# Performance work log

Measured on AMD Instinct MI355X. Metric: run time of the kernel, lower is better.

## Reference

```python
import jax, jax.numpy as jnp
import numpy as np

K = 20
HID = 64
NUM_CLASSES = 50
BIG = 1e10  # effectively-infinite distance for self-loop exclusion


def knn_idx(x, k):
    # x: [N, d] -> idx: [N, k] indices of k nearest neighbors in feature space (excluding self)
    sq = jnp.sum(x * x, axis=1)
    dist = sq[:, None] + sq[None, :] - 2.0 * (x @ x.T)  # [N, N]
    n = x.shape[0]
    dist = dist.at[jnp.arange(n), jnp.arange(n)].set(BIG)
    _, idx = jax.lax.top_k(-dist, k)
    return idx


def edge_conv(x, k, W, b):
    # DynamicEdgeConv: message = relu(Linear(cat[x_i, x_j - x_i])), aggr = max over k neighbors
    idx = knn_idx(x, k)                      # [N, k]
    xj = x[idx]                              # [N, k, d] neighbor gather
    xi = jnp.broadcast_to(x[:, None, :], xj.shape)
    feat = jnp.concatenate([xi, xj - xi], axis=-1)   # [N, k, 2d]
    h = jax.nn.relu(jnp.einsum('nkf,fo->nko', feat, W) + b)
    return jnp.max(h, axis=1)                # [N, out]


def setup_inputs() -> dict:
    key = jax.random.key(0)
    ks = jax.random.split(key, 16)
    def lin(kw, fan_in, fan_out):
        s = 1.0 / np.sqrt(fan_in)
        return jax.random.uniform(kw, (fan_in, fan_out), jnp.float32, -s, s)
    inp = {
        'x':  jax.random.normal(ks[0], (8192, 3), jnp.float32),
        'W1': lin(ks[1], 2 * 3, HID),      'b1': jnp.zeros((HID,), jnp.float32),
        'W2': lin(ks[2], 2 * HID, HID),    'b2': jnp.zeros((HID,), jnp.float32),
        'W3': lin(ks[3], 2 * HID, HID),    'b3': jnp.zeros((HID,), jnp.float32),
        'Wl': lin(ks[4], 3 * HID, 1024),   'bl': jnp.zeros((1024,), jnp.float32),
        'Wm1': lin(ks[5], 1024, 256),      'bm1': jnp.zeros((256,), jnp.float32),
        'Wm2': lin(ks[6], 256, 128),       'bm2': jnp.zeros((128,), jnp.float32),
        'Wo': lin(ks[7], 128, NUM_CLASSES),'bo': jnp.zeros((NUM_CLASSES,), jnp.float32),
    }
    return inp


def reference(x, W1, b1, W2, b2, W3, b3, Wl, bl, Wm1, bm1, Wm2, bm2, Wo, bo):
    x1 = edge_conv(x, K, W1, b1)     # [N, 64], kNN on raw 3-D points
    x2 = edge_conv(x1, K, W2, b2)    # [N, 64], kNN recomputed in feature space
    x3 = edge_conv(x2, K, W3, b3)    # [N, 64]
    h = jnp.concatenate([x1, x2, x3], axis=1)            # [N, 192]
    h = jax.nn.relu(h @ Wl + bl)                         # lin1: MLP([192, 1024])
    h = jax.nn.relu(h @ Wm1 + bm1)                       # MLP([1024, 256]) (dropout: eval mode)
    h = jax.nn.relu(h @ Wm2 + bm2)                       # MLP([256, 128])
    out = h @ Wo + bo                                    # final Linear
    return jax.nn.log_softmax(out, axis=-1)
```

## Files before the change

### kernel.cpp

```cpp
#include <hip/hip_runtime.h>
#include <math.h>

#define NPTS 8192
#define KNN 20
#define KPART 10
#define NLISTS 32

#define OFF_SQ   0
#define OFF_IDX  8192
#define OFF_A    172032
#define OFF_B    696320
#define OFF_CAT  1220608
#define OFF_H1   2793472
#define OFF_H2   11182080
#define OFF_PART OFF_H1
#define OFF_PACK (OFF_H1 + 5242880)
#define PACK_ELEMS 262144
#define OFF_WT   (OFF_H2 + 1572864)

typedef __attribute__((ext_vector_type(8))) short bf16x8;
typedef __attribute__((ext_vector_type(16))) float f32x16;

__device__ inline unsigned umed3(unsigned a, unsigned b, unsigned c) {
    unsigned d;
    asm("v_med3_u32 %0, %1, %2, %3" : "=v"(d) : "v"(a), "v"(b), "v"(c));
    return d;
}

__device__ inline unsigned short f2bf(float f) {
    unsigned u = __float_as_uint(f);
    u += 0x7FFFu + ((u >> 16) & 1u);
    return (unsigned short)(u >> 16);
}

__device__ inline void tsplit(float x, unsigned short& hi, unsigned short& lo) {
    unsigned u = __float_as_uint(x);
    hi = (unsigned short)(u >> 16);
    float d = x - __uint_as_float(u & 0xFFFF0000u);
    lo = (unsigned short)(__float_as_uint(d) >> 16);
}

__global__ __launch_bounds__(256)
void setup_kernel(const float* __restrict__ x, float* __restrict__ sq,
                  unsigned short* __restrict__ Xhi, unsigned short* __restrict__ Xlo,
                  unsigned short* __restrict__ Yhi, unsigned short* __restrict__ Ylo,
                  const float* __restrict__ Wl, const float* __restrict__ Wm1,
                  const float* __restrict__ Wm2,
                  unsigned short* __restrict__ WlT_hi, unsigned short* __restrict__ WlT_lo,
                  unsigned short* __restrict__ Wm1T_hi, unsigned short* __restrict__ Wm1T_lo,
                  unsigned short* __restrict__ Wm2T_hi, unsigned short* __restrict__ Wm2T_lo) {
    const int b = blockIdx.x;
    if (b < 1920) {
        const float* W; unsigned short *Thi, *Tlo; int t, K, nbits;
        if (b < 768)       { W = Wl;  Thi = WlT_hi;  Tlo = WlT_lo;  t = b * 256 + threadIdx.x;          K = 192;  nbits = 10; }
        else if (b < 1792) { W = Wm1; Thi = Wm1T_hi; Tlo = Wm1T_lo; t = (b - 768) * 256 + threadIdx.x;  K = 1024; nbits = 8; }
        else               { W = Wm2; Thi = Wm2T_hi; Tlo = Wm2T_lo; t = (b - 1792) * 256 + threadIdx.x; K = 256;  nbits = 7; }
        int nmask = (1 << nbits) - 1;
        int k = t >> nbits, n = t & nmask;
        float xx = W[t];
        unsigned short hi, lo;
        tsplit(xx, hi, lo);
        Thi[(size_t)n * K + k] = hi;
        Tlo[(size_t)n * K + k] = lo;
    } else if (b < 2176) {
        int t = ((b - 1920) * 256 + threadIdx.x) * 2;
        int n = t >> 4, k = t & 15;
        float xv[2];
        xv[0] = (k < 3) ? x[(size_t)n * 3 + k] : 0.f;
        xv[1] = (k + 1 < 3) ? x[(size_t)n * 3 + k + 1] : 0.f;
        ushort2 hx, lx, hy, ly;
        unsigned short* hxp = (unsigned short*)&hx;
        unsigned short* lxp = (unsigned short*)&lx;
        unsigned short* hyp = (unsigned short*)&hy;
        unsigned short* lyp = (unsigned short*)&ly;
        #pragma unroll
        for (int e = 0; e < 2; ++e) {
            float xx = xv[e];
            unsigned short hi = f2bf(xx);
            float hif = __uint_as_float((unsigned)hi << 16);
            unsigned short lo = f2bf(xx - hif);
            float y = -2.f * xx;
            unsigned short yhi = f2bf(y);
            float yhif = __uint_as_float((unsigned)yhi << 16);
            unsigned short ylo = f2bf(y - yhif);
            hxp[e] = hi; lxp[e] = lo; hyp[e] = yhi; lyp[e] = ylo;
        }
        *(ushort2*)&Xhi[t] = hx;
        *(ushort2*)&Xlo[t] = lx;
        *(ushort2*)&Yhi[t] = hy;
        *(ushort2*)&Ylo[t] = ly;
    } else {
        int n = (b - 2176) * 256 + threadIdx.x;
        float a = x[(size_t)n * 3], bb = x[(size_t)n * 3 + 1], c = x[(size_t)n * 3 + 2];
        sq[n] = fmaf(a, a, fmaf(bb, bb, c * c));
    }
}

#define NETP(key)                                                              \
    do {                                                                       \
        _Pragma("unroll")                                                      \
        for (int p = KPART - 1; p >= 1; --p)                                   \
            top[p] = umed3(key, top[p - 1], top[p]);                           \
        top[0] = min(top[0], key);                                             \
    } while (0)

#define PROCESS(Cv, j0base)                                                    \
    do {                                                                       \
        _Pragma("unroll")                                                      \
        for (int q = 0; q < 4; ++q) {                                          \
            _Pragma("unroll")                                                  \
            for (int t = 0; t < 4; ++t) {                                      \
                const int j = (j0base) + h * 4 + q * 8 + t;                    \
                float dd = fmaxf((Cv)[q * 4 + t], 0.f);                        \
                unsigned key = (__float_as_uint(dd) & 0xFFFFE000u) | (unsigned)j; \
                if (j == bi) key = 0xFFFFFFFFu;                                \
                NETP(key);                                                     \
            }                                                                  \
        }                                                                      \
    } while (0)

template<int KP>
__global__ __launch_bounds__(256, 2)
void knnA_mfma(const unsigned short* __restrict__ Yhi, const unsigned short* __restrict__ Ylo,
               const unsigned short* __restrict__ Xhi, const unsigned short* __restrict__ Xlo,
               const float* __restrict__ sq, unsigned int* __restrict__ part) {
    constexpr int NS = KP / 16;
    constexpr int NT = 8;
    const int wave = threadIdx.x >> 6, lane = threadIdx.x & 63;
    const int col = lane & 31;
    const int h   = lane >> 5;
    const int bi  = (blockIdx.x * 4 + wave) * 32 + col;
    const int jbase = blockIdx.y * 256;

    bf16x8 bhi[NS], blo[NS];
    #pragma unroll
    for (int s = 0; s < NS; ++s) {
        bhi[s] = *(const bf16x8*)&Xhi[(size_t)bi * KP + s * 16 + h * 8];
        blo[s] = *(const bf16x8*)&Xlo[(size_t)bi * KP + s * 16 + h * 8];
    }
    const float sqi = sq[bi];

    unsigned top[KPART];
    #pragma unroll
    for (int k = 0; k < KPART; ++k) top[k] = 0xFFFFFFFFu;

    bf16x8 fA[NS], fB[NS], lo[NS];
    f32x16 CCa, CCb;

    {
        const size_t a0 = (size_t)(jbase + col) * KP + h * 8;
        #pragma unroll
        for (int s = 0; s < NS; ++s)
            fA[s] = *(const bf16x8*)&Yhi[a0 + s * 16];
    }

    #pragma unroll 1
    for (int jt2 = 0; jt2 < NT; jt2 += 2) {
        const int j0 = jbase + jt2 * 32;
        const int aj = j0 + col;

        #pragma unroll
        for (int s = 0; s < NS; ++s)
            fB[s] = *(const bf16x8*)&Yhi[(size_t)(aj + 32) * KP + s * 16 + h * 8];
        #pragma unroll
        for (int s = 0; s < NS; ++s)
            lo[s] = *(const bf16x8*)&Ylo[(size_t)aj * KP + s * 16 + h * 8];
        float4 e0 = *(const float4*)&sq[j0 + h * 4];
        float4 e1 = *(const float4*)&sq[j0 + h * 4 + 8];
        float4 e2 = *(const float4*)&sq[j0 + h * 4 + 16];
        float4 e3 = *(const float4*)&sq[j0 + h * 4 + 24];

        if (jt2 > 0) PROCESS(CCb, j0 - 32);

        CCa[0] = sqi + e0.x; CCa[1] = sqi + e0.y; CCa[2]  = sqi + e0.z; CCa[3]  = sqi + e0.w;
        CCa[4] = sqi + e1.x; CCa[5] = sqi + e1.y; CCa[6]  = sqi + e1.z; CCa[7]  = sqi + e1.w;
        CCa[8] = sqi + e2.x; CCa[9] = sqi + e2.y; CCa[10] = sqi + e2.z; CCa[11] = sqi + e2.w;
        CCa[12] = sqi + e3.x; CCa[13] = sqi + e3.y; CCa[14] = sqi + e3.z; CCa[15] = sqi + e3.w;
        #pragma unroll
        for (int s = 0; s < NS; ++s) {
            CCa = __builtin_amdgcn_mfma_f32_32x32x16_bf16(fA[s], bhi[s], CCa, 0, 0, 0);
            CCa = __builtin_amdgcn_mfma_f32_32x32x16_bf16(fA[s], blo[s], CCa, 0, 0, 0);
            CCa = __builtin_amdgcn_mfma_f32_32x32x16_bf16(lo[s], bhi[s], CCa, 0, 0, 0);
        }

        if (jt2 + 2 < NT) {
            #pragma unroll
            for (int s = 0; s < NS; ++s)
                fA[s] = *(const bf16x8*)&Yhi[(size_t)(aj + 64) * KP + s * 16 + h * 8];
        }
        #pragma unroll
        for (int s = 0; s < NS; ++s)
            lo[s] = *(const bf16x8*)&Ylo[(size_t)(aj + 32) * KP + s * 16 + h * 8];
        float4 o0 = *(const float4*)&sq[j0 + 32 + h * 4];
        float4 o1 = *(const float4*)&sq[j0 + 32 + h * 4 + 8];
        float4 o2 = *(const float4*)&sq[j0 + 32 + h * 4 + 16];
        float4 o3 = *(const float4*)&sq[j0 + 32 + h * 4 + 24];

        PROCESS(CCa, j0);

        CCb[0] = sqi + o0.x; CCb[1] = sqi + o0.y; CCb[2]  = sqi + o0.z; CCb[3]  = sqi + o0.w;
        CCb[4] = sqi + o1.x; CCb[5] = sqi + o1.y; CCb[6]  = sqi + o1.z; CCb[7]  = sqi + o1.w;
        CCb[8] = sqi + o2.x; CCb[9] = sqi + o2.y; CCb[10] = sqi + o2.z; CCb[11] = sqi + o2.w;
        CCb[12] = sqi + o3.x; CCb[13] = sqi + o3.y; CCb[14] = sqi + o3.z; CCb[15] = sqi + o3.w;
        #pragma unroll
        for (int s = 0; s < NS; ++s) {
            CCb = __builtin_amdgcn_mfma_f32_32x32x16_bf16(fB[s], bhi[s], CCb, 0, 0, 0);
            CCb = __builtin_amdgcn_mfma_f32_32x32x16_bf16(fB[s], blo[s], CCb, 0, 0, 0);
            CCb = __builtin_amdgcn_mfma_f32_32x32x16_bf16(lo[s], bhi[s], CCb, 0, 0, 0);
        }
    }
    PROCESS(CCb, jbase + (NT - 1) * 32);

    {
        bool done = false;
        #pragma unroll
        for (int k = 0; k < KPART; ++k) {
            unsigned c = __shfl_xor(top[k], 32);
            if (!done) done = __all(c >= top[KPART - 1]);
            if (!done) NETP(c);
        }
    }

    if (h == 0) {
        unsigned* o = part + ((size_t)bi * NLISTS + blockIdx.y) * KPART;
        #pragma unroll
        for (int k = 0; k < KPART; ++k) o[k] = top[k];
    }
}

template<int D>
__global__ __launch_bounds__(256)
void knnBfeat_kernel(const unsigned int* __restrict__ part, int* __restrict__ idx_out,
                     const float* __restrict__ X, int stride, const float* __restrict__ W,
                     float* __restrict__ A, float* __restrict__ B) {
    const int wave = threadIdx.x >> 6, lane = threadIdx.x & 63;
    if (blockIdx.x < 1024) {
        const int half = lane >> 5;
        const int l = lane & 31;
        const int row = (blockIdx.x * 4 + wave) * 2 + half;

        unsigned top[KNN];
        const unsigned* p = part + ((size_t)row * NLISTS + l) * KPART;
        {
            uint4 v0 = *(const uint4*)(p + 0);
            uint4 v1 = *(const uint4*)(p + 4);
            uint2 v2 = *(const uint2*)(p + 8);
            top[0] = v0.x; top[1] = v0.y; top[2] = v0.z; top[3] = v0.w;
            top[4] = v1.x; top[5] = v1.y; top[6] = v1.z; top[7] = v1.w;
            top[8] = v2.x; top[9] = v2.y;
        }
        #pragma unroll
        for (int k = KPART; k < KNN; ++k) top[k] = 0xFFFFFFFFu;

        #pragma unroll
        for (int mi = 0; mi < 5; ++mi) {
            const int m = 1 << mi;
            bool done = false;
            #pragma unroll
            for (int k = 0; k < KNN; ++k) {
                unsigned c = __shfl_xor(top[k], m);
                if (!done) done = __all(c >= top[KNN - 1]);
                if (!done) {
                    #pragma unroll
                    for (int q = KNN - 1; q >= 1; --q)
                        top[q] = umed3(c, top[q - 1], top[q]);
                    top[0] = min(top[0], c);
                }
            }
        }

        if (l == 0) {
            #pragma unroll
            for (int k = 0; k < KNN; ++k)
                idx_out[(size_t)row * KNN + k] = (int)(top[k] & 0x1FFFu);
        }
    } else {
        const int n = (blockIdx.x - 1024) * 4 + wave;
        float a = 0.f, b = 0.f;
        const float* xp = X + (size_t)n * stride;
        #pragma unroll
        for (int f = 0; f < D; ++f) {
            float xf = xp[f];
            a = fmaf(xf, W[(size_t)f * 64 + lane], a);
            b = fmaf(xf, W[(size_t)(D + f) * 64 + lane], b);
        }
        A[(size_t)n * 64 + lane] = a;
        B[(size_t)n * 64 + lane] = b;
    }
}

template<bool PACKS>
__global__ __launch_bounds__(256)
void edge_fuse_kernel(const float* __restrict__ A, const float* __restrict__ B,
                      const int* __restrict__ idx, const float* __restrict__ bias,
                      float* __restrict__ out, int colofs,
                      unsigned short* __restrict__ catHi, unsigned short* __restrict__ catLo,
                      float* __restrict__ sqo,
                      unsigned short* __restrict__ Xhi, unsigned short* __restrict__ Xlo,
                      unsigned short* __restrict__ Yhi, unsigned short* __restrict__ Ylo) {
    const int wave = threadIdx.x >> 6, lane = threadIdx.x & 63;
    const int n = blockIdx.x * 4 + wave;
    const float base = A[(size_t)n * 64 + lane] - B[(size_t)n * 64 + lane] + bias[lane];
    float m = -INFINITY;
    #pragma unroll 4
    for (int k = 0; k < KNN; ++k) {
        int j = idx[(size_t)n * KNN + k];
        m = fmaxf(m, base + B[(size_t)j * 64 + lane]);
    }
    m = fmaxf(m, 0.f);
    if constexpr (PACKS) out[(size_t)n * 192 + colofs + lane] = m;

    unsigned short chi, clo;
    tsplit(m, chi, clo);
    catHi[(size_t)n * 192 + colofs + lane] = chi;
    catLo[(size_t)n * 192 + colofs + lane] = clo;

    if constexpr (PACKS) {
        float s = m * m;
        #pragma unroll
        for (int off = 32; off; off >>= 1) s += __shfl_xor(s, off);
        if (lane == 0) sqo[n] = s;

        unsigned short hi = f2bf(m);
        float hif = __uint_as_float((unsigned)hi << 16);
        unsigned short lo = f2bf(m - hif);
        float y = -2.f * m;
        unsigned short yhi = f2bf(y);
        float yhif = __uint_as_float((unsigned)yhi << 16);
        unsigned short ylo = f2bf(y - yhif);
        Xhi[(size_t)n * 64 + lane] = hi;
        Xlo[(size_t)n * 64 + lane] = lo;
        Yhi[(size_t)n * 64 + lane] = yhi;
        Ylo[(size_t)n * 64 + lane] = ylo;
    }
}

template<int K, int N, int CTW, bool SPLIT_OUT>
__global__ __launch_bounds__(256, 3)
void gemm_mfma(const unsigned short* __restrict__ Ahi, const unsigned short* __restrict__ Alo,
               const unsigned short* __restrict__ Whi, const unsigned short* __restrict__ Wlo,
               const float* __restrict__ bias, float* __restrict__ C,
               unsigned short* __restrict__ Chi, unsigned short* __restrict__ Clo) {
    const int wave = threadIdx.x >> 6, lane = threadIdx.x & 63;
    const int col = lane & 31, h = lane >> 5;
    const int r0 = blockIdx.x * 32;
    const int nb = blockIdx.y * (CTW * 128) + wave * (CTW * 32);
    const size_t abase = (size_t)(r0 + col) * K + h * 8;

    f32x16 acc[CTW];
    #pragma unroll
    for (int c = 0; c < CTW; ++c)
        #pragma unroll
        for (int r = 0; r < 16; ++r) acc[c][r] = 0.f;

    #pragma unroll 4
    for (int s = 0; s < K / 16; ++s) {
        bf16x8 ahi = *(const bf16x8*)&Ahi[abase + s * 16];
        bf16x8 alo = *(const bf16x8*)&Alo[abase + s * 16];
        #pragma unroll
        for (int c = 0; c < CTW; ++c) {
            const size_t wb = (size_t)(nb + c * 32 + col) * K + s * 16 + h * 8;
            bf16x8 bhi = *(const bf16x8*)&Whi[wb];
            bf16x8 blo = *(const bf16x8*)&Wlo[wb];
            acc[c] = __builtin_amdgcn_mfma_f32_32x32x16_bf16(ahi, bhi, acc[c], 0, 0, 0);
            acc[c] = __builtin_amdgcn_mfma_f32_32x32x16_bf16(alo, bhi, acc[c], 0, 0, 0);
            acc[c] = __builtin_amdgcn_mfma_f32_32x32x16_bf16(ahi, blo, acc[c], 0, 0, 0);
        }
    }

    #pragma unroll
    for (int c = 0; c < CTW; ++c) {
        const int n = nb + c * 32 + col;
        const float b = bias[n];
        #pragma unroll
        for (int q = 0; q < 4; ++q)
            #pragma unroll
            for (int t = 0; t < 4; ++t) {
                const int rl = 4 * h + 8 * q + t;
                float v = fmaxf(acc[c][q * 4 + t] + b, 0.f);
                if constexpr (SPLIT_OUT) {
                    unsigned short vh, vl;
                    tsplit(v, vh, vl);
                    Chi[(size_t)(r0 + rl) * N + n] = vh;
                    Clo[(size_t)(r0 + rl) * N + n] = vl;
                } else {
                    C[(size_t)(r0 + rl) * N + n] = v;
                }
            }
    }
}

__global__ __launch_bounds__(256, 2)
void gemm3f_kernel(const unsigned short* __restrict__ Ahi, const unsigned short* __restrict__ Alo,
                   const unsigned short* __restrict__ Whi, const unsigned short* __restrict__ Wlo,
                   const float* __restrict__ bias,
                   const float* __restrict__ Wo, const float* __restrict__ bo,
                   float* __restrict__ out) {
    constexpr int K = 256;
    const int wave = threadIdx.x >> 6, lane = threadIdx.x & 63;
    const int col = lane & 31, h = lane >> 5;
    const int r0 = blockIdx.x * 32;
    const int nb = wave * 32;
    const size_t abase = (size_t)(r0 + col) * K + h * 8;

    __shared__ float h3s[32][132];

    f32x16 acc;
    #pragma unroll
    for (int r = 0; r < 16; ++r) acc[r] = 0.f;

    #pragma unroll 4
    for (int s = 0; s < K / 16; ++s) {
        bf16x8 ahi = *(const bf16x8*)&Ahi[abase + s * 16];
        bf16x8 alo = *(const bf16x8*)&Alo[abase + s * 16];
        const size_t wb = (size_t)(nb + col) * K + s * 16 + h * 8;
        bf16x8 bhi = *(const bf16x8*)&Whi[wb];
        bf16x8 blo = *(const bf16x8*)&Wlo[wb];
        acc = __builtin_amdgcn_mfma_f32_32x32x16_bf16(ahi, bhi, acc, 0, 0, 0);
        acc = __builtin_amdgcn_mfma_f32_32x32x16_bf16(alo, bhi, acc, 0, 0, 0);
        acc = __builtin_amdgcn_mfma_f32_32x32x16_bf16(ahi, blo, acc, 0, 0, 0);
    }

    {
        const int n = nb + col;
        const float b = bias[n];
        #pragma unroll
        for (int q = 0; q < 4; ++q)
            #pragma unroll
            for (int t = 0; t < 4; ++t) {
                const int rl = 4 * h + 8 * q + t;
                h3s[rl][n] = fmaxf(acc[q * 4 + t] + b, 0.f);
            }
    }
    __syncthreads();

    #pragma unroll 1
    for (int rr = 0; rr < 8; ++rr) {
        const int row = wave * 8 + rr;
        float v = -INFINITY;
        if (lane < 50) {
            float a = bo[lane];
            #pragma unroll 4
            for (int f = 0; f < 128; ++f)
                a = fmaf(h3s[row][f], Wo[f * 50 + lane], a);
            v = a;
        }
        float mx = v;
        #pragma unroll
        for (int off = 32; off; off >>= 1) mx = fmaxf(mx, __shfl_xor(mx, off));
        float e = (lane < 50) ? expf(v - mx) : 0.f;
        float s = e;
        #pragma unroll
        for (int off = 32; off; off >>= 1) s += __shfl_xor(s, off);
        if (lane < 50) out[(size_t)(r0 + row) * 50 + lane] = v - mx - logf(s);
    }
}

extern "C" void kernel_launch(void* const* d_in, const int* in_sizes, int n_in,
                              void* d_out, int out_size, void* d_ws, size_t ws_size,
                              hipStream_t stream) {
    const float* x   = (const float*)d_in[0];
    const float* W1  = (const float*)d_in[1];
    const float* b1  = (const float*)d_in[2];
    const float* W2  = (const float*)d_in[3];
    const float* b2  = (const float*)d_in[4];
    const float* W3  = (const float*)d_in[5];
    const float* b3  = (const float*)d_in[6];
    const float* Wl  = (const float*)d_in[7];
    const float* bl  = (const float*)d_in[8];
    const float* Wm1 = (const float*)d_in[9];
    const float* bm1 = (const float*)d_in[10];
    const float* Wm2 = (const float*)d_in[11];
    const float* bm2 = (const float*)d_in[12];
    const float* Wo  = (const float*)d_in[13];
    const float* bo  = (const float*)d_in[14];

    float* ws   = (float*)d_ws;
    float* sq   = ws + OFF_SQ;
    int*   idx  = (int*)(ws + OFF_IDX);
    float* Abuf = ws + OFF_A;
    float* Bbuf = ws + OFF_B;
    float* cat  = ws + OFF_CAT;
    unsigned int* part = (unsigned int*)(ws + OFF_PART);
    unsigned short* Phi = (unsigned short*)(ws + OFF_PACK);
    unsigned short* Plo = (unsigned short*)(ws + OFF_PACK + PACK_ELEMS);
    unsigned short* Qhi = (unsigned short*)(ws + OFF_PACK + 2 * PACK_ELEMS);
    unsigned short* Qlo = (unsigned short*)(ws + OFF_PACK + 3 * PACK_ELEMS);
    unsigned short* h1hi = (unsigned short*)(ws + OFF_H1);
    unsigned short* h1lo = (unsigned short*)(ws + OFF_H1 + 4194304);
    unsigned short* catHi = (unsigned short*)(ws + OFF_H2);
    unsigned short* catLo = (unsigned short*)(ws + OFF_H2 + 786432);
    unsigned short* h2hi = (unsigned short*)(ws + OFF_A);
    unsigned short* h2lo = (unsigned short*)(ws + OFF_CAT);
    unsigned short* WlT_hi  = (unsigned short*)(ws + OFF_WT);
    unsigned short* WlT_lo  = (unsigned short*)(ws + OFF_WT + 98304);
    unsigned short* Wm1T_hi = (unsigned short*)(ws + OFF_WT + 196608);
    unsigned short* Wm1T_lo = (unsigned short*)(ws + OFF_WT + 327680);
    unsigned short* Wm2T_hi = (unsigned short*)(ws + OFF_WT + 458752);
    unsigned short* Wm2T_lo = (unsigned short*)(ws + OFF_WT + 475136);
    float* out  = (float*)d_out;

    dim3 b256(256);
    dim3 gknn(64, 32);

    setup_kernel<<<2208, b256, 0, stream>>>(x, sq, Phi, Plo, Qhi, Qlo,
                                            Wl, Wm1, Wm2, WlT_hi, WlT_lo,
                                            Wm1T_hi, Wm1T_lo, Wm2T_hi, Wm2T_lo);

    knnA_mfma<16><<<gknn, b256, 0, stream>>>(Qhi, Qlo, Phi, Plo, sq, part);
    knnBfeat_kernel<3><<<3072, b256, 0, stream>>>(part, idx, x, 3, W1, Abuf, Bbuf);
    edge_fuse_kernel<true><<<2048, b256, 0, stream>>>(Abuf, Bbuf, idx, b1, cat, 0,
                                                      catHi, catLo, sq, Phi, Plo, Qhi, Qlo);

    knnA_mfma<64><<<gknn, b256, 0, stream>>>(Qhi, Qlo, Phi, Plo, sq, part);
    knnBfeat_kernel<64><<<3072, b256, 0, stream>>>(part, idx, cat, 192, W2, Abuf, Bbuf);
    edge_fuse_kernel<true><<<2048, b256, 0, stream>>>(Abuf, Bbuf, idx, b2, cat, 64,
                                                      catHi, catLo, sq, Phi, Plo, Qhi, Qlo);

    knnA_mfma<64><<<gknn, b256, 0, stream>>>(Qhi, Qlo, Phi, Plo, sq, part);
    knnBfeat_kernel<64><<<3072, b256, 0, stream>>>(part, idx, cat + 64, 192, W3, Abuf, Bbuf);
    edge_fuse_kernel<false><<<2048, b256, 0, stream>>>(Abuf, Bbuf, idx, b3, cat, 128,
                                                       catHi, catLo, nullptr,
                                                       nullptr, nullptr, nullptr, nullptr);

    dim3 g1(256, 4);
    gemm_mfma<192, 1024, 2, true><<<g1, b256, 0, stream>>>(catHi, catLo, WlT_hi, WlT_lo,
                                                           bl, nullptr, h1hi, h1lo);
    dim3 g2(256, 2);
    gemm_mfma<1024, 256, 1, true><<<g2, b256, 0, stream>>>(h1hi, h1lo, Wm1T_hi, Wm1T_lo,
                                                           bm1, nullptr, h2hi, h2lo);
    gemm3f_kernel<<<256, b256, 0, stream>>>(h2hi, h2lo, Wm2T_hi, Wm2T_lo,
                                            bm2, Wo, bo, out);
}
```

Baseline: 440.9 us.

## Drop double-buffered kNN tile pipeline and raise occupancy to eight blocks

Replaces the manually software-pipelined two-accumulator loop in the MFMA kNN distance kernel with a simple one-tile-per-iteration loop that loads A fragments inline. The launch bound minimum blocks per CU is raised from 2 to 8, forcing fewer registers per thread. The aim is to hide memory latency through more resident waves rather than explicit prefetch overlap between MFMA and the top-k sorting network. The risk is register spilling under the tighter budget and the loss of explicit overlap between loads, MFMA and selection.

After: 596.4 us. 1.35x slower.

```diff
diff --git a/kernel.cpp b/kernel.cpp
--- a/kernel.cpp
+++ b/kernel.cpp
@@ -120,7 +120,7 @@
     } while (0)
 
 template<int KP>
-__global__ __launch_bounds__(256, 2)
+__global__ __launch_bounds__(256, 8)
 void knnA_mfma(const unsigned short* __restrict__ Yhi, const unsigned short* __restrict__ Ylo,
                const unsigned short* __restrict__ Xhi, const unsigned short* __restrict__ Xlo,
                const float* __restrict__ sq, unsigned int* __restrict__ part) {
@@ -144,72 +144,29 @@
     #pragma unroll
     for (int k = 0; k < KPART; ++k) top[k] = 0xFFFFFFFFu;
 
-    bf16x8 fA[NS], fB[NS], lo[NS];
-    f32x16 CCa, CCb;
-
-    {
-        const size_t a0 = (size_t)(jbase + col) * KP + h * 8;
-        #pragma unroll
-        for (int s = 0; s < NS; ++s)
-            fA[s] = *(const bf16x8*)&Yhi[a0 + s * 16];
-    }
-
     #pragma unroll 1
-    for (int jt2 = 0; jt2 < NT; jt2 += 2) {
-        const int j0 = jbase + jt2 * 32;
+    for (int jt = 0; jt < NT; ++jt) {
+        const int j0 = jbase + jt * 32;
         const int aj = j0 + col;
-
-        #pragma unroll
-        for (int s = 0; s < NS; ++s)
-            fB[s] = *(const bf16x8*)&Yhi[(size_t)(aj + 32) * KP + s * 16 + h * 8];
-        #pragma unroll
-        for (int s = 0; s < NS; ++s)
-            lo[s] = *(const bf16x8*)&Ylo[(size_t)aj * KP + s * 16 + h * 8];
-        float4 e0 = *(const float4*)&sq[j0 + h * 4];
-        float4 e1 = *(const float4*)&sq[j0 + h * 4 + 8];
-        float4 e2 = *(const float4*)&sq[j0 + h * 4 + 16];
-        float4 e3 = *(const float4*)&sq[j0 + h * 4 + 24];
-
-        if (jt2 > 0) PROCESS(CCb, j0 - 32);
-
-        CCa[0] = sqi + e0.x; CCa[1] = sqi + e0.y; CCa[2]  = sqi + e0.z; CCa[3]  = sqi + e0.w;
-        CCa[4] = sqi + e1.x; CCa[5] = sqi + e1.y; CCa[6]  = sqi + e1.z; CCa[7]  = sqi + e1.w;
-        CCa[8] = sqi + e2.x; CCa[9] = sqi + e2.y; CCa[10] = sqi + e2.z; CCa[11] = sqi + e2.w;
-        CCa[12] = sqi + e3.x; CCa[13] = sqi + e3.y; CCa[14] = sqi + e3.z; CCa[15] = sqi + e3.w;
+        f32x16 C;
+        #pragma unroll
+        for (int q = 0; q < 4; ++q) {
+            const float4 s4 = *(const float4*)&sq[j0 + h * 4 + q * 8];
+            C[q * 4 + 0] = sqi + s4.x;
+            C[q * 4 + 1] = sqi + s4.y;
+            C[q * 4 + 2] = sqi + s4.z;
+            C[q * 4 + 3] = sqi + s4.w;
+        }
         #pragma unroll
         for (int s = 0; s < NS; ++s) {
-            CCa = __builtin_amdgcn_mfma_f32_32x32x16_bf16(fA[s], bhi[s], CCa, 0, 0, 0);
-            CCa = __builtin_amdgcn_mfma_f32_32x32x16_bf16(fA[s], blo[s], CCa, 0, 0, 0);
-            CCa = __builtin_amdgcn_mfma_f32_32x32x16_bf16(lo[s], bhi[s], CCa, 0, 0, 0);
-        }
-
-        if (jt2 + 2 < NT) {
-            #pragma unroll
-            for (int s = 0; s < NS; ++s)
-                fA[s] = *(const bf16x8*)&Yhi[(size_t)(aj + 64) * KP + s * 16 + h * 8];
-        }
-        #pragma unroll
-        for (int s = 0; s < NS; ++s)
-            lo[s] = *(const bf16x8*)&Ylo[(size_t)(aj + 32) * KP + s * 16 + h * 8];
-        float4 o0 = *(const float4*)&sq[j0 + 32 + h * 4];
-        float4 o1 = *(const float4*)&sq[j0 + 32 + h * 4 + 8];
-        float4 o2 = *(const float4*)&sq[j0 + 32 + h * 4 + 16];
-        float4 o3 = *(const float4*)&sq[j0 + 32 + h * 4 + 24];
-
-        PROCESS(CCa, j0);
-
-        CCb[0] = sqi + o0.x; CCb[1] = sqi + o0.y; CCb[2]  = sqi + o0.z; CCb[3]  = sqi + o0.w;
-        CCb[4] = sqi + o1.x; CCb[5] = sqi + o1.y; CCb[6]  = sqi + o1.z; CCb[7]  = sqi + o1.w;
-        CCb[8] = sqi + o2.x; CCb[9] = sqi + o2.y; CCb[10] = sqi + o2.z; CCb[11] = sqi + o2.w;
-        CCb[12] = sqi + o3.x; CCb[13] = sqi + o3.y; CCb[14] = sqi + o3.z; CCb[15] = sqi + o3.w;
-        #pragma unroll
-        for (int s = 0; s < NS; ++s) {
-            CCb = __builtin_amdgcn_mfma_f32_32x32x16_bf16(fB[s], bhi[s], CCb, 0, 0, 0);
-            CCb = __builtin_amdgcn_mfma_f32_32x32x16_bf16(fB[s], blo[s], CCb, 0, 0, 0);
-            CCb = __builtin_amdgcn_mfma_f32_32x32x16_bf16(lo[s], bhi[s], CCb, 0, 0, 0);
-        }
-    }
-    PROCESS(CCb, jbase + (NT - 1) * 32);
+            bf16x8 ahi = *(const bf16x8*)&Yhi[(size_t)aj * KP + s * 16 + h * 8];
+            bf16x8 alo = *(const bf16x8*)&Ylo[(size_t)aj * KP + s * 16 + h * 8];
+            C = __builtin_amdgcn_mfma_f32_32x32x16_bf16(ahi, bhi[s], C, 0, 0, 0);
+            C = __builtin_amdgcn_mfma_f32_32x32x16_bf16(ahi, blo[s], C, 0, 0, 0);
+            C = __builtin_amdgcn_mfma_f32_32x32x16_bf16(alo, bhi[s], C, 0, 0, 0);
+        }
+        PROCESS(C, j0);
+    }
 
     {
         bool done = false;
```

## Use 16x16x32 MFMA kNN distance kernel for 64-dim feature layers

Applied to the files above, without the earlier changes.

Adds a new kNN partial top-k kernel built on 16x16x32 bf16 MFMA tiles, with 16 query rows per wave and 256 candidate columns per block. Each lane keeps a per-row top-10 list, and the lists are merged across lane groups with shuffles. The kernel replaces the existing 32-wide MFMA kNN kernel for layers 2 and 3 and uses twice as many blocks in x. The aim is a smaller per-wave accumulator, higher occupancy and more parallelism. The cost is that candidate rows are reloaded from global memory for every 16-column tile, and a second shuffle merge round is needed.

Result: slower. 549.9 us (+24.7%).

```diff
diff --git a/kernel.cpp b/kernel.cpp
--- a/kernel.cpp
+++ b/kernel.cpp
@@ -20,6 +20,7 @@
 
 typedef __attribute__((ext_vector_type(8))) short bf16x8;
 typedef __attribute__((ext_vector_type(16))) float f32x16;
+typedef __attribute__((ext_vector_type(4))) float f32x4;
 
 __device__ inline unsigned umed3(unsigned a, unsigned b, unsigned c) {
     unsigned d;
@@ -228,6 +229,74 @@
     }
 }
 
+__global__ __launch_bounds__(256, 2)
+void knnA16_mfma(const unsigned short* __restrict__ Yhi, const unsigned short* __restrict__ Ylo,
+                 const unsigned short* __restrict__ Xhi, const unsigned short* __restrict__ Xlo,
+                 const float* __restrict__ sq, unsigned int* __restrict__ part) {
+    constexpr int KP = 64;
+    constexpr int NS = 2;
+    const int wave = threadIdx.x >> 6, lane = threadIdx.x & 63;
+    const int c16 = lane & 15;
+    const int g   = lane >> 4;
+    const int bi  = (blockIdx.x * 4 + wave) * 16 + c16;
+    const int jbase = blockIdx.y * 256;
+
+    bf16x8 bhi[NS], blo[NS];
+    #pragma unroll
+    for (int s = 0; s < NS; ++s) {
+        bhi[s] = *(const bf16x8*)&Xhi[(size_t)bi * KP + s * 32 + g * 8];
+        blo[s] = *(const bf16x8*)&Xlo[(size_t)bi * KP + s * 32 + g * 8];
+    }
+    const float sqi = sq[bi];
+
+    unsigned top[KPART];
+    #pragma unroll
+    for (int k = 0; k < KPART; ++k) top[k] = 0xFFFFFFFFu;
+
+    #pragma unroll 1
+    for (int jt = 0; jt < 16; ++jt) {
+        const int j0 = jbase + jt * 16;
+        const int aj = j0 + c16;
+        f32x4 C;
+        const float4 s4 = *(const float4*)&sq[j0 + g * 4];
+        C[0] = sqi + s4.x; C[1] = sqi + s4.y; C[2] = sqi + s4.z; C[3] = sqi + s4.w;
+        #pragma unroll
+        for (int s = 0; s < NS; ++s) {
+            bf16x8 ahi = *(const bf16x8*)&Yhi[(size_t)aj * KP + s * 32 + g * 8];
+            bf16x8 alo = *(const bf16x8*)&Ylo[(size_t)aj * KP + s * 32 + g * 8];
+            C = __builtin_amdgcn_mfma_f32_16x16x32_bf16(ahi, bhi[s], C, 0, 0, 0);
+            C = __builtin_amdgcn_mfma_f32_16x16x32_bf16(ahi, blo[s], C, 0, 0, 0);
+            C = __builtin_amdgcn_mfma_f32_16x16x32_bf16(alo, bhi[s], C, 0, 0, 0);
+        }
+        #pragma unroll
+        for (int t = 0; t < 4; ++t) {
+            const int j = j0 + g * 4 + t;
+            float dd = fmaxf(C[t], 0.f);
+            unsigned key = (__float_as_uint(dd) & 0xFFFFE000u) | (unsigned)j;
+            if (j == bi) key = 0xFFFFFFFFu;
+            NETP(key);
+        }
+    }
+
+    #pragma unroll
+    for (int mi = 0; mi < 2; ++mi) {
+        const int mm = 16 << mi;
+        bool done = false;
+        #pragma unroll
+        for (int k = 0; k < KPART; ++k) {
+            unsigned c = __shfl_xor(top[k], mm);
+            if (!done) done = __all(c >= top[KPART - 1]);
+            if (!done) NETP(c);
+        }
+    }
+
+    if (lane < 16) {
+        unsigned* o = part + ((size_t)bi * NLISTS + blockIdx.y) * KPART;
+        #pragma unroll
+        for (int k = 0; k < KPART; ++k) o[k] = top[k];
+    }
+}
+
 template<int D>
 __global__ __launch_bounds__(256)
 void knnBfeat_kernel(const unsigned int* __restrict__ part, int* __restrict__ idx_out,
@@ -502,6 +571,7 @@
 
     dim3 b256(256);
     dim3 gknn(64, 32);
+    dim3 gknn16(128, 32);
 
     setup_kernel<<<2208, b256, 0, stream>>>(x, sq, Phi, Plo, Qhi, Qlo,
                                             Wl, Wm1, Wm2, WlT_hi, WlT_lo,
@@ -512,12 +582,12 @@
     edge_fuse_kernel<true><<<2048, b256, 0, stream>>>(Abuf, Bbuf, idx, b1, cat, 0,
                                                       catHi, catLo, sq, Phi, Plo, Qhi, Qlo);
 
-    knnA_mfma<64><<<gknn, b256, 0, stream>>>(Qhi, Qlo, Phi, Plo, sq, part);
+    knnA16_mfma<<<gknn16, b256, 0, stream>>>(Qhi, Qlo, Phi, Plo, sq, part);
     knnBfeat_kernel<64><<<3072, b256, 0, stream>>>(part, idx, cat, 192, W2, Abuf, Bbuf);
     edge_fuse_kernel<true><<<2048, b256, 0, stream>>>(Abuf, Bbuf, idx, b2, cat, 64,
                                                       catHi, catLo, sq, Phi, Plo, Qhi, Qlo);
 
-    knnA_mfma<64><<<gknn, b256, 0, stream>>>(Qhi, Qlo, Phi, Plo, sq, part);
+    knnA16_mfma<<<gknn16, b256, 0, stream>>>(Qhi, Qlo, Phi, Plo, sq, part);
     knnBfeat_kernel<64><<<3072, b256, 0, stream>>>(part, idx, cat + 64, 192, W3, Abuf, Bbuf);
     edge_fuse_kernel<false><<<2048, b256, 0, stream>>>(Abuf, Bbuf, idx, b3, cat, 128,
                                                        catHi, catLo, nullptr,
```
